# Optimization experiments

Hardware: AMD Instinct MI355X
Metric: run time of the kernel (lower is better)

The kernel has to match this reference:

```python
import jax, jax.numpy as jnp
import numpy as np

BATCH = 8192
MAX_PIECES = 32
NNZ = BATCH * MAX_PIECES
FT_OUT = 512
N_FEATURES = 768


def setup_inputs() -> dict:
    key = jax.random.key(0)
    ks = jax.random.split(key, 8)
    # COO indices: row 0 = batch index (each position contributes MAX_PIECES features),
    # row 1 = feature index in [0, 768)
    batch_ids = jnp.repeat(jnp.arange(BATCH, dtype=jnp.int64), MAX_PIECES)
    stm_feat = jax.random.randint(ks[0], (NNZ,), 0, N_FEATURES, dtype=jnp.int64)
    nstm_feat = jax.random.randint(ks[1], (NNZ,), 0, N_FEATURES, dtype=jnp.int64)
    stm_indices = jnp.stack([batch_ids, stm_feat])   # [2, nnz]
    nstm_indices = jnp.stack([batch_ids, nstm_feat])  # [2, nnz]
    values = jnp.ones((NNZ,), dtype=jnp.float32)      # binary features
    # Linear(768, FT_OUT): store weight transposed as [768, FT_OUT]
    ft_w = jax.random.normal(ks[2], (N_FEATURES, FT_OUT), dtype=jnp.float32) * (1.0 / np.sqrt(N_FEATURES))
    ft_b = jax.random.normal(ks[3], (FT_OUT,), dtype=jnp.float32) * 0.01
    # Linear(2*FT_OUT, 1): stored as [2*FT_OUT, 1]
    out_w = jax.random.normal(ks[4], (2 * FT_OUT, 1), dtype=jnp.float32) * (1.0 / np.sqrt(2 * FT_OUT))
    out_b = jax.random.normal(ks[5], (1,), dtype=jnp.float32) * 0.01
    return {
        "stm_indices": stm_indices,
        "nstm_indices": nstm_indices,
        "values": values,
        "ft_w": ft_w,
        "ft_b": ft_b,
        "out_w": out_w,
        "out_b": out_b,
        "batch_size": BATCH,
    }


def reference(stm_indices, nstm_indices, values, ft_w, ft_b, out_w, out_b, batch_size):
    def feature_transform(indices):
        # sparse @ W^T + b  ==  gather rows of W^T by feature id, scale by value,
        # segment-sum into batch rows. rows: [nnz, FT_OUT]
        rows = ft_w[indices[1]] * values[:, None]
        acc = jax.ops.segment_sum(rows, indices[0], num_segments=batch_size)
        return acc + ft_b

    stm_ft = feature_transform(stm_indices)    # [B, FT_OUT]
    nstm_ft = feature_transform(nstm_indices)  # [B, FT_OUT]
    hidden = jnp.clip(jnp.concatenate([stm_ft, nstm_ft], axis=1), 0.0, 1.0)
    return jax.nn.sigmoid(hidden @ out_w + out_b)  # [B, 1]
```

## Files before the change

### kernel.cpp

```cpp
#include <hip/hip_runtime.h>
#include <math.h>

#define MAX_PIECES 32
#define FT_OUT 512
#define N_FEATURES 768

__global__ __launch_bounds__(256) void cvt_bf16(
    const float* __restrict__ ft_w, unsigned short* __restrict__ wtab, int n)
{
    const int i = (blockIdx.x * 256 + threadIdx.x) * 4;
    if (i >= n) return;
    const float4 f = *(const float4*)(ft_w + i);
    ushort4 o;
    const float vf[4] = {f.x, f.y, f.z, f.w};
    unsigned short ov[4];
    #pragma unroll
    for (int j = 0; j < 4; ++j) {
        unsigned int u = __float_as_uint(vf[j]);
        u += 0x7fffu + ((u >> 16) & 1u);
        ov[j] = (unsigned short)(u >> 16);
    }
    o.x = ov[0]; o.y = ov[1]; o.z = ov[2]; o.w = ov[3];
    *(ushort4*)(wtab + i) = o;
}

__global__ __launch_bounds__(256) void nnue_fwd(
    const int*   __restrict__ stm_idx,
    const int*   __restrict__ nstm_idx,
    const float* __restrict__ values,
    const unsigned short* __restrict__ wtab,
    const float* __restrict__ ft_b,
    const float* __restrict__ out_w,
    const float* __restrict__ out_b,
    float*       __restrict__ out,
    int nnz)
{
    const int t    = threadIdx.x;
    const int g    = t >> 6;
    const int lane = t & 63;
    const int rb   = g >> 1;
    const int side = g & 1;
    const int row  = blockIdx.x * 2 + rb;

    __shared__ int   s_idx[4][MAX_PIECES];
    __shared__ float s_val[2][MAX_PIECES];
    __shared__ float s_red[4];

    if (t < 128) {
        const int lg = t >> 5, li = t & 31;
        const int lrow = blockIdx.x * 2 + (lg >> 1);
        const int* src = (lg & 1) ? nstm_idx : stm_idx;
        s_idx[lg][li] = src[nnz + lrow * MAX_PIECES + li];
    } else if (t < 192) {
        const int lrb = (t >> 5) & 1, li = t & 31;
        const int lrow = blockIdx.x * 2 + lrb;
        s_val[lrb][li] = values[lrow * MAX_PIECES + li];
    }
    __syncthreads();

    float acc[8];
    #pragma unroll
    for (int j = 0; j < 8; ++j) acc[j] = 0.f;

    const int colbase = lane * 8;

    #pragma unroll
    for (int i = 0; i < MAX_PIECES; ++i) {
        const int   feat = s_idx[g][i];
        const float v    = s_val[rb][i];
        const uint4 u = *(const uint4*)(wtab + feat * FT_OUT + colbase);
        const unsigned int uw[4] = {u.x, u.y, u.z, u.w};
        #pragma unroll
        for (int k = 0; k < 4; ++k) {
            const float lo = __uint_as_float(uw[k] << 16);
            const float hi = __uint_as_float(uw[k] & 0xffff0000u);
            acc[2 * k]     = fmaf(lo, v, acc[2 * k]);
            acc[2 * k + 1] = fmaf(hi, v, acc[2 * k + 1]);
        }
    }

    const float4 b0 = *(const float4*)(ft_b + colbase);
    const float4 b1 = *(const float4*)(ft_b + colbase + 4);
    const float bb[8] = {b0.x, b0.y, b0.z, b0.w, b1.x, b1.y, b1.z, b1.w};
    const float4 w0 = *(const float4*)(out_w + side * FT_OUT + colbase);
    const float4 w1 = *(const float4*)(out_w + side * FT_OUT + colbase + 4);
    const float ww[8] = {w0.x, w0.y, w0.z, w0.w, w1.x, w1.y, w1.z, w1.w};

    float p = 0.f;
    #pragma unroll
    for (int j = 0; j < 8; ++j) {
        const float h = fminf(fmaxf(acc[j] + bb[j], 0.f), 1.f);
        p = fmaf(h, ww[j], p);
    }

    #pragma unroll
    for (int off = 32; off > 0; off >>= 1)
        p += __shfl_down(p, off, 64);
    if (lane == 0) s_red[g] = p;
    __syncthreads();

    if (t < 2) {
        const float s = s_red[2 * t] + s_red[2 * t + 1] + out_b[0];
        out[blockIdx.x * 2 + t] = 1.f / (1.f + expf(-s));
    }
}

extern "C" void kernel_launch(void* const* d_in, const int* in_sizes, int n_in,
                              void* d_out, int out_size, void* d_ws, size_t ws_size,
                              hipStream_t stream) {
    const int*   stm_idx  = (const int*)d_in[0];
    const int*   nstm_idx = (const int*)d_in[1];
    const float* values   = (const float*)d_in[2];
    const float* ft_w     = (const float*)d_in[3];
    const float* ft_b     = (const float*)d_in[4];
    const float* out_w    = (const float*)d_in[5];
    const float* out_b    = (const float*)d_in[6];
    float*       out      = (float*)d_out;

    const int nnz = in_sizes[0] / 2;
    const int B   = out_size;
    const int nw  = N_FEATURES * FT_OUT;

    unsigned short* wtab = (unsigned short*)d_ws;

    cvt_bf16<<<(nw / 4 + 255) / 256, 256, 0, stream>>>(ft_w, wtab, nw);
    nnue_fwd<<<B / 2, 256, 0, stream>>>(stm_idx, nstm_idx, values, wtab,
                                        ft_b, out_w, out_b, out, nnz);
}
```

Measured before the change: 90.96 us.

## Stage per-slice bf16 weight columns in LDS and gather from shared memory

The kernel now splits the 512 output columns into 64-column slices. Each 1024-thread block copies its full 768x64 bf16 weight slice into LDS once, then processes 256 batch rows in chunks of 32, gathering feature rows from LDS instead of L2. Each slice's partial dot product with the output weights is reduced within the wave and added to a per-row accumulator with atomics, and a separate head kernel applies the bias and sigmoid. The aim is to replace repeated global/L2 gathers with much faster LDS reads. In exchange it adds a memset, an extra kernel launch, float atomics whose summation order is nondeterministic, and roughly 96KB of LDS per block, which limits occupancy.

```diff
diff --git a/kernel.cpp b/kernel.cpp
--- a/kernel.cpp
+++ b/kernel.cpp
@@ -3,7 +3,13 @@
 
 #define MAX_PIECES 32
 #define FT_OUT 512
-#define N_FEATURES 768
+#define NFEAT 768
+#define SLICE_COLS 64
+#define NSLICE (FT_OUT / SLICE_COLS)
+#define ROWS_PER_BLOCK 256
+#define CHUNK_ROWS 32
+#define NCHUNK (ROWS_PER_BLOCK / CHUNK_ROWS)
+#define THREADS 1024
 
 __global__ __launch_bounds__(256) void cvt_bf16(
     const float* __restrict__ ft_w, unsigned short* __restrict__ wtab, int n)
@@ -11,7 +17,6 @@
     const int i = (blockIdx.x * 256 + threadIdx.x) * 4;
     if (i >= n) return;
     const float4 f = *(const float4*)(ft_w + i);
-    ushort4 o;
     const float vf[4] = {f.x, f.y, f.z, f.w};
     unsigned short ov[4];
     #pragma unroll
@@ -20,89 +25,114 @@
         u += 0x7fffu + ((u >> 16) & 1u);
         ov[j] = (unsigned short)(u >> 16);
     }
-    o.x = ov[0]; o.y = ov[1]; o.z = ov[2]; o.w = ov[3];
+    ushort4 o; o.x = ov[0]; o.y = ov[1]; o.z = ov[2]; o.w = ov[3];
     *(ushort4*)(wtab + i) = o;
 }
 
-__global__ __launch_bounds__(256) void nnue_fwd(
+__global__ __launch_bounds__(THREADS) void nnue_gather(
     const int*   __restrict__ stm_idx,
     const int*   __restrict__ nstm_idx,
     const float* __restrict__ values,
     const unsigned short* __restrict__ wtab,
     const float* __restrict__ ft_b,
     const float* __restrict__ out_w,
-    const float* __restrict__ out_b,
-    float*       __restrict__ out,
+    float*       __restrict__ acc_out,
     int nnz)
 {
+    const int s    = blockIdx.x & (NSLICE - 1);
+    const int grp  = blockIdx.x >> 3;
     const int t    = threadIdx.x;
-    const int g    = t >> 6;
     const int lane = t & 63;
-    const int rb   = g >> 1;
-    const int side = g & 1;
-    const int row  = blockIdx.x * 2 + rb;
+    const int w    = t >> 6;
+    const int cg   = lane & 15;
+    const int fg   = lane >> 4;
+    const int colb = cg * 4;
+    const int side = w & 1;
 
-    __shared__ int   s_idx[4][MAX_PIECES];
-    __shared__ float s_val[2][MAX_PIECES];
-    __shared__ float s_red[4];
+    __shared__ unsigned short s_w[NFEAT][SLICE_COLS];
+    __shared__ int   s_idx[2][CHUNK_ROWS][MAX_PIECES];
+    __shared__ float s_val[CHUNK_ROWS][MAX_PIECES];
+    __shared__ float s_b[SLICE_COLS];
+    __shared__ float s_hw[2][SLICE_COLS];
 
-    if (t < 128) {
-        const int lg = t >> 5, li = t & 31;
-        const int lrow = blockIdx.x * 2 + (lg >> 1);
-        const int* src = (lg & 1) ? nstm_idx : stm_idx;
-        s_idx[lg][li] = src[nnz + lrow * MAX_PIECES + li];
-    } else if (t < 192) {
-        const int lrb = (t >> 5) & 1, li = t & 31;
-        const int lrow = blockIdx.x * 2 + lrb;
-        s_val[lrb][li] = values[lrow * MAX_PIECES + li];
+    #pragma unroll
+    for (int k = 0; k < (NFEAT * SLICE_COLS / 8) / THREADS; ++k) {
+        const int id = k * THREADS + t;
+        const int r = id >> 3, c8 = id & 7;
+        const uint4 u = *(const uint4*)(wtab + r * FT_OUT + s * SLICE_COLS + c8 * 8);
+        *(uint4*)(&s_w[r][c8 * 8]) = u;
+    }
+    if (t < SLICE_COLS) {
+        s_b[t] = ft_b[s * SLICE_COLS + t];
+    } else if (t < 2 * SLICE_COLS) {
+        s_hw[0][t - 64] = out_w[s * SLICE_COLS + (t - 64)];
+    } else if (t < 3 * SLICE_COLS) {
+        s_hw[1][t - 128] = out_w[FT_OUT + s * SLICE_COLS + (t - 128)];
     }
     __syncthreads();
 
-    float acc[8];
+    float bias[4], hws[4];
     #pragma unroll
-    for (int j = 0; j < 8; ++j) acc[j] = 0.f;
-
-    const int colbase = lane * 8;
-
-    #pragma unroll
-    for (int i = 0; i < MAX_PIECES; ++i) {
-        const int   feat = s_idx[g][i];
-        const float v    = s_val[rb][i];
-        const uint4 u = *(const uint4*)(wtab + feat * FT_OUT + colbase);
-        const unsigned int uw[4] = {u.x, u.y, u.z, u.w};
-        #pragma unroll
-        for (int k = 0; k < 4; ++k) {
-            const float lo = __uint_as_float(uw[k] << 16);
-            const float hi = __uint_as_float(uw[k] & 0xffff0000u);
-            acc[2 * k]     = fmaf(lo, v, acc[2 * k]);
-            acc[2 * k + 1] = fmaf(hi, v, acc[2 * k + 1]);
-        }
+    for (int j = 0; j < 4; ++j) {
+        bias[j] = s_b[colb + j];
+        hws[j]  = side ? s_hw[1][colb + j] : s_hw[0][colb + j];
     }
 
-    const float4 b0 = *(const float4*)(ft_b + colbase);
-    const float4 b1 = *(const float4*)(ft_b + colbase + 4);
-    const float bb[8] = {b0.x, b0.y, b0.z, b0.w, b1.x, b1.y, b1.z, b1.w};
-    const float4 w0 = *(const float4*)(out_w + side * FT_OUT + colbase);
-    const float4 w1 = *(const float4*)(out_w + side * FT_OUT + colbase + 4);
-    const float ww[8] = {w0.x, w0.y, w0.z, w0.w, w1.x, w1.y, w1.z, w1.w};
+    const int row0 = grp * ROWS_PER_BLOCK;
 
-    float p = 0.f;
-    #pragma unroll
-    for (int j = 0; j < 8; ++j) {
-        const float h = fminf(fmaxf(acc[j] + bb[j], 0.f), 1.f);
-        p = fmaf(h, ww[j], p);
+    for (int chunk = 0; chunk < NCHUNK; ++chunk) {
+        const int crow0 = row0 + chunk * CHUNK_ROWS;
+
+        {
+            const int rc = t >> 5, pc = t & 31;
+            const int gi = (crow0 + rc) * MAX_PIECES + pc;
+            s_idx[0][rc][pc] = stm_idx[nnz + gi];
+            s_idx[1][rc][pc] = nstm_idx[nnz + gi];
+            s_val[rc][pc]    = values[gi];
+        }
+        __syncthreads();
+
+        #pragma unroll
+        for (int qi = 0; qi < 4; ++qi) {
+            const int rc = qi * 8 + (w >> 1);
+            float a0 = 0.f, a1 = 0.f, a2 = 0.f, a3 = 0.f;
+            #pragma unroll
+            for (int k = 0; k < 8; ++k) {
+                const int   f = s_idx[side][rc][fg + 4 * k];
+                const float v = s_val[rc][fg + 4 * k];
+                const uint2 u = *(const uint2*)(&s_w[f][colb]);
+                a0 = fmaf(__uint_as_float(u.x << 16),          v, a0);
+                a1 = fmaf(__uint_as_float(u.x & 0xffff0000u),  v, a1);
+                a2 = fmaf(__uint_as_float(u.y << 16),          v, a2);
+                a3 = fmaf(__uint_as_float(u.y & 0xffff0000u),  v, a3);
+            }
+            a0 += __shfl_xor(a0, 16, 64); a0 += __shfl_xor(a0, 32, 64);
+            a1 += __shfl_xor(a1, 16, 64); a1 += __shfl_xor(a1, 32, 64);
+            a2 += __shfl_xor(a2, 16, 64); a2 += __shfl_xor(a2, 32, 64);
+            a3 += __shfl_xor(a3, 16, 64); a3 += __shfl_xor(a3, 32, 64);
+
+            float p;
+            p = fminf(fmaxf(a0 + bias[0], 0.f), 1.f) * hws[0];
+            p = fmaf(fminf(fmaxf(a1 + bias[1], 0.f), 1.f), hws[1], p);
+            p = fmaf(fminf(fmaxf(a2 + bias[2], 0.f), 1.f), hws[2], p);
+            p = fmaf(fminf(fmaxf(a3 + bias[3], 0.f), 1.f), hws[3], p);
+
+            #pragma unroll
+            for (int off = 1; off < 64; off <<= 1)
+                p += __shfl_xor(p, off, 64);
+            if (lane == 0)
+                atomicAdd(&acc_out[crow0 + rc], 0.25f * p);
+        }
+        __syncthreads();
     }
+}
 
-    #pragma unroll
-    for (int off = 32; off > 0; off >>= 1)
-        p += __shfl_down(p, off, 64);
-    if (lane == 0) s_red[g] = p;
-    __syncthreads();
-
-    if (t < 2) {
-        const float s = s_red[2 * t] + s_red[2 * t + 1] + out_b[0];
-        out[blockIdx.x * 2 + t] = 1.f / (1.f + expf(-s));
-    }
+__global__ __launch_bounds__(256) void nnue_head(
+    const float* __restrict__ acc, const float* __restrict__ out_b,
+    float* __restrict__ out, int B)
+{
+    const int i = blockIdx.x * 256 + threadIdx.x;
+    if (i < B) out[i] = 1.f / (1.f + expf(-(acc[i] + out_b[0])));
 }
 
 extern "C" void kernel_launch(void* const* d_in, const int* in_sizes, int n_in,
@@ -119,11 +149,14 @@
 
     const int nnz = in_sizes[0] / 2;
     const int B   = out_size;
-    const int nw  = N_FEATURES * FT_OUT;
+    const int nw  = NFEAT * FT_OUT;
 
-    unsigned short* wtab = (unsigned short*)d_ws;
+    float*          acc  = (float*)d_ws;
+    unsigned short* wtab = (unsigned short*)((char*)d_ws + (1 << 20));
 
+    hipMemsetAsync(acc, 0, B * sizeof(float), stream);
     cvt_bf16<<<(nw / 4 + 255) / 256, 256, 0, stream>>>(ft_w, wtab, nw);
-    nnue_fwd<<<B / 2, 256, 0, stream>>>(stm_idx, nstm_idx, values, wtab,
-                                        ft_b, out_w, out_b, out, nnz);
+    nnue_gather<<<NSLICE * (B / ROWS_PER_BLOCK), THREADS, 0, stream>>>(
+        stm_idx, nstm_idx, values, wtab, ft_b, out_w, acc, nnz);
+    nnue_head<<<(B + 255) / 256, 256, 0, stream>>>(acc, out_b, out, B);
 }
```

Result: slower. 121.1 us (+33.1%).
